# Performance work log

Measured on AMD Instinct MI355X. Metric: run time of the kernel, lower is better.

## Reference

```python
import jax, jax.numpy as jnp
import numpy as np

N = 50000
E = 1600000
D_CONTENT, D_STYLE, D_CAT = 768, 128, 32  # concat feature = 2*D_CAT = 64
H1, H2, NCLS = 64, 64, 2


def _lin_params(key, din, dout, bias=True):
    k1, k2 = jax.random.split(key)
    s = 1.0 / np.sqrt(din)
    W = jax.random.uniform(k1, (din, dout), jnp.float32, -s, s)
    b = jax.random.uniform(k2, (dout,), jnp.float32, -s, s) if bias else None
    return W, b


def setup_inputs() -> dict:
    key = jax.random.key(0)
    ks = jax.random.split(key, 16)
    x_content = jax.random.normal(ks[0], (N, D_CONTENT), jnp.float32)
    x_style = jax.random.normal(ks[1], (N, D_STYLE), jnp.float32)
    edge_index = jax.random.randint(ks[2], (2, E), 0, N, jnp.int64)
    edge_type = jax.random.randint(ks[3], (E,), 0, 4, jnp.int64)
    Wp, bp = _lin_params(ks[4], D_CONTENT, D_CAT)
    Ws, bs = _lin_params(ks[5], D_STYLE, D_CAT)
    # SAGEConv: lin_l (aggregated neighbors, has bias), lin_r (root, no bias)
    Wl1, bl1 = _lin_params(ks[6], 2 * D_CAT, H1)
    Wr1, _ = _lin_params(ks[7], 2 * D_CAT, H1, bias=False)
    Wl2, bl2 = _lin_params(ks[8], H1, H2)
    Wr2, _ = _lin_params(ks[9], H1, H2, bias=False)
    Wl3, bl3 = _lin_params(ks[10], H2, H2)
    Wr3, _ = _lin_params(ks[11], H2, H2, bias=False)
    Wo, bo = _lin_params(ks[12], H2, NCLS)
    return dict(x_content=x_content, x_style=x_style, edge_index=edge_index,
                edge_type=edge_type, Wp=Wp, bp=bp, Ws=Ws, bs=bs,
                Wl1=Wl1, bl1=bl1, Wr1=Wr1, Wl2=Wl2, bl2=bl2, Wr2=Wr2,
                Wl3=Wl3, bl3=bl3, Wr3=Wr3, Wo=Wo, bo=bo)


def _sage_conv(x, src, dst, Wl, bl, Wr):
    # mean aggregation of source-node features at destination nodes
    msg_sum = jax.ops.segment_sum(x[src], dst, num_segments=N)  # [N, d]
    deg = jax.ops.segment_sum(jnp.ones((src.shape[0],), x.dtype), dst,
                              num_segments=N)
    agg = msg_sum / jnp.maximum(deg, 1.0)[:, None]
    return agg @ Wl + bl + x @ Wr


def reference(x_content, x_style, edge_index, edge_type,
              Wp, bp, Ws, bs, Wl1, bl1, Wr1, Wl2, bl2, Wr2,
              Wl3, bl3, Wr3, Wo, bo):
    src, dst = edge_index[0], edge_index[1]
    x = jnp.concatenate([x_content @ Wp + bp, x_style @ Ws + bs], axis=1)
    x = jax.nn.relu(_sage_conv(x, src, dst, Wl1, bl1, Wr1))  # dropout = id (eval)
    x = jax.nn.relu(_sage_conv(x, src, dst, Wl2, bl2, Wr2))
    x = jax.nn.relu(_sage_conv(x, src, dst, Wl3, bl3, Wr3))
    return x @ Wo + bo
```

## Files before the change

kernel.cpp:

```cpp
#include <hip/hip_runtime.h>
#include <stdint.h>


typedef __attribute__((ext_vector_type(8))) unsigned short u16x8;
typedef __attribute__((ext_vector_type(4))) float f32x4;
typedef __attribute__((ext_vector_type(4))) unsigned int u32x4;
typedef __attribute__((ext_vector_type(2))) int i32x2;

static __device__ __forceinline__ float bf2f(unsigned short u) {
  union { unsigned int i; float f; } v;
  v.i = ((unsigned int)u) << 16;
  return v.f;
}

static __device__ __forceinline__ unsigned short f2bf(float f) {
  union { float f; unsigned int i; } v;
  v.f = f;
  unsigned int u = v.i;
  unsigned int r = (u + 0x7FFFu + ((u >> 16) & 1u)) >> 16;
  return (unsigned short)r;
}

template <bool BF>
static __device__ __forceinline__ float ldf(const void* p, long long i) {
  if (BF) return bf2f(((const unsigned short*)p)[i]);
  return ((const float*)p)[i];
}

static __device__ __forceinline__ int clampN(int v, int N) {
  return v < 0 ? 0 : (v >= N ? N - 1 : v);
}

__global__ void k_detect(const void* Wp, const int* ei, int* flags) {
  if (threadIdx.x == 0 && blockIdx.x == 0) {
    const unsigned short* w = (const unsigned short*)Wp;
    int bf = 1;
    for (int i = 0; i < 64; ++i) {
      float v = fabsf(bf2f(w[i]));
      if (!(v < 1.0f)) bf = 0;
    }
    flags[0] = bf;
    int i64 = 1;
    for (int i = 0; i < 32; ++i)
      if (ei[2 * i + 1] != 0) i64 = 0;
    flags[1] = i64;
  }
}

static __device__ __forceinline__ int edge_src(const int* ei, int e, int E,
                                               int i64) {
  return i64 ? ei[2 * (long long)e] : ei[e];
}
static __device__ __forceinline__ int edge_dst(const int* ei, int e, int E,
                                               int i64) {
  return i64 ? ei[2 * ((long long)E + e)] : ei[(long long)E + e];
}


__global__ __launch_bounds__(256) void k_pack(const int* __restrict__ ei, int E,
                                              int N, int* __restrict__ cnt,
                                              i32x2* __restrict__ pairs,
                                              const int* __restrict__ flags) {
  int e = blockIdx.x * 256 + threadIdx.x;
  if (e < E) {
    int i64 = flags[1];
    int s = clampN(edge_src(ei, e, E, i64), N);
    int d = clampN(edge_dst(ei, e, E, i64), N);
    i32x2 p;
    p[0] = s;
    p[1] = d;
    pairs[e] = p;
    atomicAdd(&cnt[d], 1);
  }
}

__global__ __launch_bounds__(256) void k_scan1(const int* __restrict__ cnt,
                                               int* __restrict__ rowptr,
                                               int* __restrict__ bsum, int N) {
  __shared__ int sh[256];
  int t = threadIdx.x;
  int base = blockIdx.x * 1024 + t * 4;
  int v0 = 0, v1 = 0, v2 = 0, v3 = 0;
  if (base + 0 < N) v0 = cnt[base + 0];
  if (base + 1 < N) v1 = cnt[base + 1];
  if (base + 2 < N) v2 = cnt[base + 2];
  if (base + 3 < N) v3 = cnt[base + 3];
  int s = v0 + v1 + v2 + v3;
  sh[t] = s;
  __syncthreads();
  int acc = s;
  for (int off = 1; off < 256; off <<= 1) {
    int x = 0;
    if (t >= off) x = sh[t - off];
    __syncthreads();
    acc += x;
    sh[t] = acc;
    __syncthreads();
  }
  int run = acc - s;
  if (base + 0 < N) rowptr[base + 0] = run;
  run += v0;
  if (base + 1 < N) rowptr[base + 1] = run;
  run += v1;
  if (base + 2 < N) rowptr[base + 2] = run;
  run += v2;
  if (base + 3 < N) rowptr[base + 3] = run;
  run += v3;
  if (t == 255) bsum[blockIdx.x] = acc;
}

__global__ void k_scan2(int* __restrict__ bsum, int nb,
                        int* __restrict__ rowptr, int N) {
  if (threadIdx.x == 0 && blockIdx.x == 0) {
    int run = 0;
    for (int i = 0; i < nb; ++i) {
      int v = bsum[i];
      bsum[i] = run;
      run += v;
    }
    rowptr[N] = run;
  }
}

__global__ __launch_bounds__(256) void k_scan3(int* __restrict__ rowptr,
                                               int* __restrict__ cursor,
                                               const int* __restrict__ bsum,
                                               int N) {
  int i = blockIdx.x * 256 + threadIdx.x;
  if (i < N) {
    int v = rowptr[i] + bsum[i >> 10];
    rowptr[i] = v;
    cursor[i] = v;
  }
}

__global__ __launch_bounds__(256) void k_scatter2(
    const i32x2* __restrict__ pairs, int E, int lo, int hi,
    int* __restrict__ cursor, int* __restrict__ colbuf) {
  int e = blockIdx.x * 256 + threadIdx.x;
  if (e < E) {
    i32x2 p2 = pairs[e];
    int d = p2[1];
    if (d >= lo && d < hi) {
      int p = atomicAdd(&cursor[d], 1);
      if (p >= 0 && p < E) colbuf[p] = p2[0];
    }
  }
}

template <bool BF>
static __device__ void project_body(const void* __restrict__ xc,
                                    const void* __restrict__ xs,
                                    const void* __restrict__ Wp,
                                    const void* __restrict__ bp,
                                    const void* __restrict__ Ws,
                                    const void* __restrict__ bs,
                                    float* __restrict__ h0, int N,
                                    float* __restrict__ lds) {
  float* xt = lds;
  unsigned int* wtb = (unsigned int*)(lds + 2 * 64 * 68);
  float* wtf = lds + 2 * 64 * 68;

  int tid = (int)threadIdx.x;
  int w = __builtin_amdgcn_readfirstlane(tid >> 6);
  int lane = tid & 63;
  int node = (int)blockIdx.x * 64 + lane;

  int sn = tid >> 2;
  int sj = tid & 3;
  int gsn = (int)blockIdx.x * 64 + sn;
  int gsnc = gsn < N ? gsn : (N - 1);

  float c[8], s[8];
#pragma unroll
  for (int r = 0; r < 8; ++r) {
    c[r] = 0.f;
    s[r] = 0.f;
  }

  u16x8 pr0 = {}, pr1 = {};
  f32x4 pf0 = {}, pf1 = {}, pf2 = {}, pf3 = {};
  u32x4 wrg = {};
  f32x4 wf0 = {}, wf1 = {};

  auto stage_load = [&](int t) {
    long long idx;
    const void* src;
    if (t < 12) {
      src = xc;
      idx = (long long)gsnc * 768 + t * 64 + 16 * sj;
    } else {
      src = xs;
      idx = (long long)gsnc * 128 + (t - 12) * 64 + 16 * sj;
    }
    if (BF) {
      const unsigned short* p = (const unsigned short*)src + idx;
      pr0 = *(const u16x8*)p;
      pr1 = *(const u16x8*)(p + 8);
    } else {
      const float* p = (const float*)src + idx;
      pf0 = *(const f32x4*)(p + 0);
      pf1 = *(const f32x4*)(p + 4);
      pf2 = *(const f32x4*)(p + 8);
      pf3 = *(const f32x4*)(p + 12);
    }
    int rowg = (t < 12) ? (t * 64 + sn) : ((t - 12) * 64 + sn);
    const void* wsrc = (t < 12) ? Wp : Ws;
    if (BF) {
      wrg = *(const u32x4*)((const unsigned int*)wsrc +
                            (long long)rowg * 16 + 4 * sj);
    } else {
      const float* p = (const float*)wsrc + (long long)rowg * 32 + 8 * sj;
      wf0 = *(const f32x4*)p;
      wf1 = *(const f32x4*)(p + 4);
    }
  };

  auto stage_write = [&](int t) {
    float* row = xt + (t & 1) * (64 * 68) + sn * 68 + 16 * sj;
    if (BF) {
      f32x4 v;
#pragma unroll
      for (int i = 0; i < 4; ++i) v[i] = bf2f(pr0[i]);
      *(f32x4*)(row + 0) = v;
#pragma unroll
      for (int i = 0; i < 4; ++i) v[i] = bf2f(pr0[4 + i]);
      *(f32x4*)(row + 4) = v;
#pragma unroll
      for (int i = 0; i < 4; ++i) v[i] = bf2f(pr1[i]);
      *(f32x4*)(row + 8) = v;
#pragma unroll
      for (int i = 0; i < 4; ++i) v[i] = bf2f(pr1[4 + i]);
      *(f32x4*)(row + 12) = v;
    } else {
      *(f32x4*)(row + 0) = pf0;
      *(f32x4*)(row + 4) = pf1;
      *(f32x4*)(row + 8) = pf2;
      *(f32x4*)(row + 12) = pf3;
    }
    if (BF) {
      *(u32x4*)(wtb + (t & 1) * (64 * 16) + sn * 16 + 4 * sj) = wrg;
    } else {
      float* wrow = wtf + (t & 1) * (64 * 32) + sn * 32 + 8 * sj;
      *(f32x4*)wrow = wf0;
      *(f32x4*)(wrow + 4) = wf1;
    }
  };

  stage_load(0);
  stage_write(0);
  __syncthreads();

#pragma unroll 1
  for (int t = 0; t < 14; ++t) {
    if (t + 1 < 14) stage_load(t + 1);

    const float* xrow = xt + (t & 1) * (64 * 68) + lane * 68;
    if (BF) {
      const unsigned int* wbase = wtb + (t & 1) * (64 * 16) + 4 * w;
      if (t < 12) {
#pragma unroll 2
        for (int k0 = 0; k0 < 64; k0 += 4) {
          f32x4 x4 = *(const f32x4*)(xrow + k0);
#pragma unroll
          for (int kk = 0; kk < 4; ++kk) {
            u32x4 wp4 = *(const u32x4*)(wbase + (k0 + kk) * 16);
#pragma unroll
            for (int p = 0; p < 4; ++p) {
              union { unsigned int i; float f; } lo, hi;
              lo.i = wp4[p] << 16;
              hi.i = wp4[p] & 0xFFFF0000u;
              c[2 * p + 0] += x4[kk] * lo.f;
              c[2 * p + 1] += x4[kk] * hi.f;
            }
          }
        }
      } else {
#pragma unroll 2
        for (int k0 = 0; k0 < 64; k0 += 4) {
          f32x4 x4 = *(const f32x4*)(xrow + k0);
#pragma unroll
          for (int kk = 0; kk < 4; ++kk) {
            u32x4 wp4 = *(const u32x4*)(wbase + (k0 + kk) * 16);
#pragma unroll
            for (int p = 0; p < 4; ++p) {
              union { unsigned int i; float f; } lo, hi;
              lo.i = wp4[p] << 16;
              hi.i = wp4[p] & 0xFFFF0000u;
              s[2 * p + 0] += x4[kk] * lo.f;
              s[2 * p + 1] += x4[kk] * hi.f;
            }
          }
        }
      }
    } else {
      const float* wbase = wtf + (t & 1) * (64 * 32) + 8 * w;
      if (t < 12) {
#pragma unroll 2
        for (int k0 = 0; k0 < 64; k0 += 4) {
          f32x4 x4 = *(const f32x4*)(xrow + k0);
#pragma unroll
          for (int kk = 0; kk < 4; ++kk) {
            const float* wr = wbase + (k0 + kk) * 32;
            f32x4 wa = *(const f32x4*)wr;
            f32x4 wb = *(const f32x4*)(wr + 4);
#pragma unroll
            for (int r = 0; r < 4; ++r) {
              c[r] += x4[kk] * wa[r];
              c[4 + r] += x4[kk] * wb[r];
            }
          }
        }
      } else {
#pragma unroll 2
        for (int k0 = 0; k0 < 64; k0 += 4) {
          f32x4 x4 = *(const f32x4*)(xrow + k0);
#pragma unroll
          for (int kk = 0; kk < 4; ++kk) {
            const float* wr = wbase + (k0 + kk) * 32;
            f32x4 wa = *(const f32x4*)wr;
            f32x4 wb = *(const f32x4*)(wr + 4);
#pragma unroll
            for (int r = 0; r < 4; ++r) {
              s[r] += x4[kk] * wa[r];
              s[4 + r] += x4[kk] * wb[r];
            }
          }
        }
      }
    }

    if (t + 1 < 14) stage_write(t + 1);
    __syncthreads();
  }

  if (node < N) {
    float* orow = h0 + (long long)node * 64;
    f32x4 v;
#pragma unroll
    for (int r = 0; r < 4; ++r) v[r] = c[r] + ldf<BF>(bp, 8 * w + r);
    *(f32x4*)(orow + 8 * w) = v;
#pragma unroll
    for (int r = 0; r < 4; ++r) v[r] = c[4 + r] + ldf<BF>(bp, 8 * w + 4 + r);
    *(f32x4*)(orow + 8 * w + 4) = v;
#pragma unroll
    for (int r = 0; r < 4; ++r) v[r] = s[r] + ldf<BF>(bs, 8 * w + r);
    *(f32x4*)(orow + 32 + 8 * w) = v;
#pragma unroll
    for (int r = 0; r < 4; ++r) v[r] = s[4 + r] + ldf<BF>(bs, 8 * w + 4 + r);
    *(f32x4*)(orow + 32 + 8 * w + 4) = v;
  }
}

__global__ __launch_bounds__(256) void k_project(
    const void* __restrict__ xc, const void* __restrict__ xs,
    const void* __restrict__ Wp, const void* __restrict__ bp,
    const void* __restrict__ Ws, const void* __restrict__ bs,
    float* __restrict__ h0, int N, const int* __restrict__ flags) {
  __shared__ float lds[2 * 64 * 68 + 2 * 64 * 32];
  if (flags[0])
    project_body<true>(xc, xs, Wp, bp, Ws, bs, h0, N, lds);
  else
    project_body<false>(xc, xs, Wp, bp, Ws, bs, h0, N, lds);
}

template <bool BF>
static __device__ void layer_body(const float* __restrict__ hin,
                                  const int* __restrict__ rowptr,
                                  const int* __restrict__ colbuf,
                                  const void* Wl, const void* bl,
                                  const void* Wr, float* __restrict__ hout,
                                  int N, int last, const void* Wo,
                                  const void* bo, void* outp) {
  int node = (int)((blockIdx.x * blockDim.x + threadIdx.x) >> 6);
  int lane = (int)(threadIdx.x & 63);
  if (node >= N) return;
  int rs = rowptr[node], re = rowptr[node + 1];
  float xself = hin[(long long)node * 64 + lane];
  float agg0 = 0.f, agg1 = 0.f, agg2 = 0.f, agg3 = 0.f;
  float agg4 = 0.f, agg5 = 0.f, agg6 = 0.f, agg7 = 0.f;
  for (int cb = rs; cb < re; cb += 64) {
    int sidx = 0;
    if (cb + lane < re) sidx = clampN(colbuf[cb + lane], N);
    int c = re - cb;
    if (c > 64) c = 64;
    int t = 0;
    for (; t + 8 <= c; t += 8) {
      int s0 = __builtin_amdgcn_readlane(sidx, t + 0);
      int s1 = __builtin_amdgcn_readlane(sidx, t + 1);
      int s2 = __builtin_amdgcn_readlane(sidx, t + 2);
      int s3 = __builtin_amdgcn_readlane(sidx, t + 3);
      int s4 = __builtin_amdgcn_readlane(sidx, t + 4);
      int s5 = __builtin_amdgcn_readlane(sidx, t + 5);
      int s6 = __builtin_amdgcn_readlane(sidx, t + 6);
      int s7 = __builtin_amdgcn_readlane(sidx, t + 7);
      float v0 = hin[(long long)s0 * 64 + lane];
      float v1 = hin[(long long)s1 * 64 + lane];
      float v2 = hin[(long long)s2 * 64 + lane];
      float v3 = hin[(long long)s3 * 64 + lane];
      float v4 = hin[(long long)s4 * 64 + lane];
      float v5 = hin[(long long)s5 * 64 + lane];
      float v6 = hin[(long long)s6 * 64 + lane];
      float v7 = hin[(long long)s7 * 64 + lane];
      agg0 += v0;
      agg1 += v1;
      agg2 += v2;
      agg3 += v3;
      agg4 += v4;
      agg5 += v5;
      agg6 += v6;
      agg7 += v7;
    }
    for (; t < c; ++t) {
      int s = __builtin_amdgcn_readlane(sidx, t);
      agg0 += hin[(long long)s * 64 + lane];
    }
  }
  float agg = ((agg0 + agg1) + (agg2 + agg3)) + ((agg4 + agg5) + (agg6 + agg7));
  int deg = re - rs;
  if (deg > 0) agg *= (1.f / (float)deg);

  float o = ldf<BF>(bl, lane);
#pragma unroll 8
  for (int d = 0; d < 64; ++d) {
    float ad = __uint_as_float(
        __builtin_amdgcn_readlane(__float_as_uint(agg), d));
    float xd = __uint_as_float(
        __builtin_amdgcn_readlane(__float_as_uint(xself), d));
    o += ad * ldf<BF>(Wl, d * 64 + lane);
    o += xd * ldf<BF>(Wr, d * 64 + lane);
  }
  o = fmaxf(o, 0.f);

  if (!last) {
    hout[(long long)node * 64 + lane] = o;
  } else {
    float c0 = o * ldf<BF>(Wo, lane * 2 + 0);
    float c1 = o * ldf<BF>(Wo, lane * 2 + 1);
    for (int off = 32; off > 0; off >>= 1) {
      c0 += __shfl_xor(c0, off, 64);
      c1 += __shfl_xor(c1, off, 64);
    }
    if (lane == 0) {
      float r0 = c0 + ldf<BF>(bo, 0);
      float r1 = c1 + ldf<BF>(bo, 1);
      if (BF) {
        unsigned short* o16 = (unsigned short*)outp;
        o16[(long long)node * 2 + 0] = f2bf(r0);
        o16[(long long)node * 2 + 1] = f2bf(r1);
      } else {
        float* o32 = (float*)outp;
        o32[(long long)node * 2 + 0] = r0;
        o32[(long long)node * 2 + 1] = r1;
      }
    }
  }
}

__global__ __launch_bounds__(256) void k_layer(
    const float* hin, const int* rowptr, const int* colbuf, const void* Wl,
    const void* bl, const void* Wr, float* hout, int N, int last,
    const void* Wo, const void* bo, void* outp, const int* __restrict__ flags) {
  if (flags[0])
    layer_body<true>(hin, rowptr, colbuf, Wl, bl, Wr, hout, N, last, Wo, bo,
                     outp);
  else
    layer_body<false>(hin, rowptr, colbuf, Wl, bl, Wr, hout, N, last, Wo, bo,
                      outp);
}


extern "C" void kernel_launch(void* const* d_in, const int* in_sizes, int n_in,
                              void* d_out, int out_size, void* d_ws,
                              size_t ws_size, hipStream_t stream) {
  const void* xc = d_in[0];
  const void* xs = d_in[1];
  const int* ei = (const int*)d_in[2];
  const void* Wp = d_in[4];
  const void* bp = d_in[5];
  const void* Ws = d_in[6];
  const void* bs = d_in[7];
  const void* Wl1 = d_in[8];
  const void* bl1 = d_in[9];
  const void* Wr1 = d_in[10];
  const void* Wl2 = d_in[11];
  const void* bl2 = d_in[12];
  const void* Wr2 = d_in[13];
  const void* Wl3 = d_in[14];
  const void* bl3 = d_in[15];
  const void* Wr3 = d_in[16];
  const void* Wo = d_in[17];
  const void* bo = d_in[18];

  int N = out_size / 2;
  int E = in_sizes[3];

  char* ws = (char*)d_ws;
  size_t off = 0;
  auto alloc = [&](size_t bytes) {
    char* p = ws + off;
    off += (bytes + 255) & ~(size_t)255;
    return p;
  };
  int* colbuf = (int*)alloc((size_t)E * 4);
  int* cnt = (int*)alloc((size_t)N * 4);
  int* rowptr = (int*)alloc((size_t)(N + 1) * 4);
  int* cursor = (int*)alloc((size_t)N * 4);
  int* bsum = (int*)alloc(4096);
  int* flags = (int*)alloc(256);
  float* h0 = (float*)alloc((size_t)N * 64 * 4);
  float* h1 = (float*)alloc((size_t)N * 64 * 4);
  (void)ws_size;
  (void)n_in;

  i32x2* pairs = (i32x2*)h0;

  k_detect<<<1, 64, 0, stream>>>(Wp, ei, flags);

  hipMemsetAsync(cnt, 0, (size_t)N * 4, stream);
  int eb = (E + 255) / 256;
  k_pack<<<eb, 256, 0, stream>>>(ei, E, N, cnt, pairs, flags);
  int sb = (N + 1023) / 1024;
  k_scan1<<<sb, 256, 0, stream>>>(cnt, rowptr, bsum, N);
  k_scan2<<<1, 64, 0, stream>>>(bsum, sb, rowptr, N);
  k_scan3<<<(N + 255) / 256, 256, 0, stream>>>(rowptr, cursor, bsum, N);

  const int NPASS = 8;
  int chunk = (N + NPASS - 1) / NPASS;
  for (int r = 0; r < NPASS; ++r) {
    int lo = r * chunk;
    int hi = lo + chunk < N ? lo + chunk : N;
    k_scatter2<<<eb, 256, 0, stream>>>(pairs, E, lo, hi, cursor, colbuf);
  }

  int pb = (N + 63) / 64;
  k_project<<<pb, 256, 0, stream>>>(xc, xs, Wp, bp, Ws, bs, h0, N, flags);

  int nb4 = (N + 3) / 4;
  k_layer<<<nb4, 256, 0, stream>>>(h0, rowptr, colbuf, Wl1, bl1, Wr1, h1, N, 0,
                                   nullptr, nullptr, nullptr, flags);
  k_layer<<<nb4, 256, 0, stream>>>(h1, rowptr, colbuf, Wl2, bl2, Wr2, h0, N, 0,
                                   nullptr, nullptr, nullptr, flags);
  k_layer<<<nb4, 256, 0, stream>>>(h0, rowptr, colbuf, Wl3, bl3, Wr3, h1, N, 1,
                                   Wo, bo, d_out, flags);
}
```

Baseline: 730.2 us.

## Split projection K-range across two blocks, widen gather unroll, halve scatter passes

```diff
diff --git a/kernel.cpp b/kernel.cpp
--- a/kernel.cpp
+++ b/kernel.cpp
@@ -152,10 +152,9 @@
 static __device__ void project_body(const void* __restrict__ xc,
                                     const void* __restrict__ xs,
                                     const void* __restrict__ Wp,
-                                    const void* __restrict__ bp,
                                     const void* __restrict__ Ws,
-                                    const void* __restrict__ bs,
-                                    float* __restrict__ h0, int N,
+                                    float* __restrict__ pout, int N,
+                                    int nb0, int tile_lo, int tile_hi,
                                     float* __restrict__ lds) {
   float* xt = lds;
   unsigned int* wtb = (unsigned int*)(lds + 2 * 64 * 68);
@@ -164,11 +163,11 @@
   int tid = (int)threadIdx.x;
   int w = __builtin_amdgcn_readfirstlane(tid >> 6);
   int lane = tid & 63;
-  int node = (int)blockIdx.x * 64 + lane;
+  int node = nb0 * 64 + lane;
 
   int sn = tid >> 2;
   int sj = tid & 3;
-  int gsn = (int)blockIdx.x * 64 + sn;
+  int gsn = nb0 * 64 + sn;
   int gsnc = gsn < N ? gsn : (N - 1);
 
   float c[8], s[8];
@@ -247,13 +246,13 @@
     }
   };
 
-  stage_load(0);
-  stage_write(0);
+  stage_load(tile_lo);
+  stage_write(tile_lo);
   __syncthreads();
 
 #pragma unroll 1
-  for (int t = 0; t < 14; ++t) {
-    if (t + 1 < 14) stage_load(t + 1);
+  for (int t = tile_lo; t < tile_hi; ++t) {
+    if (t + 1 < tile_hi) stage_load(t + 1);
 
     const float* xrow = xt + (t & 1) * (64 * 68) + lane * 68;
     if (BF) {
@@ -330,38 +329,75 @@
       }
     }
 
-    if (t + 1 < 14) stage_write(t + 1);
+    if (t + 1 < tile_hi) stage_write(t + 1);
     __syncthreads();
   }
 
   if (node < N) {
-    float* orow = h0 + (long long)node * 64;
+    float* orow = pout + (long long)node * 64;
     f32x4 v;
 #pragma unroll
-    for (int r = 0; r < 4; ++r) v[r] = c[r] + ldf<BF>(bp, 8 * w + r);
+    for (int r = 0; r < 4; ++r) v[r] = c[r];
     *(f32x4*)(orow + 8 * w) = v;
 #pragma unroll
-    for (int r = 0; r < 4; ++r) v[r] = c[4 + r] + ldf<BF>(bp, 8 * w + 4 + r);
+    for (int r = 0; r < 4; ++r) v[r] = c[4 + r];
     *(f32x4*)(orow + 8 * w + 4) = v;
 #pragma unroll
-    for (int r = 0; r < 4; ++r) v[r] = s[r] + ldf<BF>(bs, 8 * w + r);
+    for (int r = 0; r < 4; ++r) v[r] = s[r];
     *(f32x4*)(orow + 32 + 8 * w) = v;
 #pragma unroll
-    for (int r = 0; r < 4; ++r) v[r] = s[4 + r] + ldf<BF>(bs, 8 * w + 4 + r);
+    for (int r = 0; r < 4; ++r) v[r] = s[4 + r];
     *(f32x4*)(orow + 32 + 8 * w + 4) = v;
   }
 }
 
 __global__ __launch_bounds__(256) void k_project(
     const void* __restrict__ xc, const void* __restrict__ xs,
-    const void* __restrict__ Wp, const void* __restrict__ bp,
-    const void* __restrict__ Ws, const void* __restrict__ bs,
-    float* __restrict__ h0, int N, const int* __restrict__ flags) {
+    const void* __restrict__ Wp, const void* __restrict__ Ws,
+    float* __restrict__ p0, float* __restrict__ p1, int N,
+    const int* __restrict__ flags) {
   __shared__ float lds[2 * 64 * 68 + 2 * 64 * 32];
+  int b = (int)blockIdx.x;
+  int nb0 = b >> 1;
+  int half = b & 1;
+  float* pout = half ? p1 : p0;
+  int tlo = half * 7, thi = half * 7 + 7;
   if (flags[0])
-    project_body<true>(xc, xs, Wp, bp, Ws, bs, h0, N, lds);
+    project_body<true>(xc, xs, Wp, Ws, pout, N, nb0, tlo, thi, lds);
   else
-    project_body<false>(xc, xs, Wp, bp, Ws, bs, h0, N, lds);
+    project_body<false>(xc, xs, Wp, Ws, pout, N, nb0, tlo, thi, lds);
+}
+
+template <bool BF>
+static __device__ void combine_body(float* __restrict__ p0,
+                                    const float* __restrict__ p1,
+                                    const void* __restrict__ bp,
+                                    const void* __restrict__ bs, int N) {
+  long long i = (long long)blockIdx.x * 256 + threadIdx.x;
+  long long tot = (long long)N * 16;
+  if (i < tot) {
+    int oc = (int)((i & 15) * 4);
+    f32x4 a = *(f32x4*)(p0 + i * 4);
+    f32x4 b = *(const f32x4*)(p1 + i * 4);
+    f32x4 v;
+#pragma unroll
+    for (int r = 0; r < 4; ++r) {
+      int col = oc + r;
+      float bias = (col < 32) ? ldf<BF>(bp, col) : ldf<BF>(bs, col - 32);
+      v[r] = a[r] + b[r] + bias;
+    }
+    *(f32x4*)(p0 + i * 4) = v;
+  }
+}
+
+__global__ __launch_bounds__(256) void k_combine(
+    float* __restrict__ p0, const float* __restrict__ p1,
+    const void* __restrict__ bp, const void* __restrict__ bs, int N,
+    const int* __restrict__ flags) {
+  if (flags[0])
+    combine_body<true>(p0, p1, bp, bs, N);
+  else
+    combine_body<false>(p0, p1, bp, bs, N);
 }
 
 template <bool BF>
@@ -385,6 +421,48 @@
     int c = re - cb;
     if (c > 64) c = 64;
     int t = 0;
+    for (; t + 16 <= c; t += 16) {
+      int s0 = __builtin_amdgcn_readlane(sidx, t + 0);
+      int s1 = __builtin_amdgcn_readlane(sidx, t + 1);
+      int s2 = __builtin_amdgcn_readlane(sidx, t + 2);
+      int s3 = __builtin_amdgcn_readlane(sidx, t + 3);
+      int s4 = __builtin_amdgcn_readlane(sidx, t + 4);
+      int s5 = __builtin_amdgcn_readlane(sidx, t + 5);
+      int s6 = __builtin_amdgcn_readlane(sidx, t + 6);
+      int s7 = __builtin_amdgcn_readlane(sidx, t + 7);
+      int s8 = __builtin_amdgcn_readlane(sidx, t + 8);
+      int s9 = __builtin_amdgcn_readlane(sidx, t + 9);
+      int sa = __builtin_amdgcn_readlane(sidx, t + 10);
+      int sb = __builtin_amdgcn_readlane(sidx, t + 11);
+      int sc = __builtin_amdgcn_readlane(sidx, t + 12);
+      int sd = __builtin_amdgcn_readlane(sidx, t + 13);
+      int se = __builtin_amdgcn_readlane(sidx, t + 14);
+      int sf = __builtin_amdgcn_readlane(sidx, t + 15);
+      float v0 = hin[(long long)s0 * 64 + lane];
+      float v1 = hin[(long long)s1 * 64 + lane];
+      float v2 = hin[(long long)s2 * 64 + lane];
+      float v3 = hin[(long long)s3 * 64 + lane];
+      float v4 = hin[(long long)s4 * 64 + lane];
+      float v5 = hin[(long long)s5 * 64 + lane];
+      float v6 = hin[(long long)s6 * 64 + lane];
+      float v7 = hin[(long long)s7 * 64 + lane];
+      float v8 = hin[(long long)s8 * 64 + lane];
+      float v9 = hin[(long long)s9 * 64 + lane];
+      float va = hin[(long long)sa * 64 + lane];
+      float vb = hin[(long long)sb * 64 + lane];
+      float vc = hin[(long long)sc * 64 + lane];
+      float vd = hin[(long long)sd * 64 + lane];
+      float ve = hin[(long long)se * 64 + lane];
+      float vf = hin[(long long)sf * 64 + lane];
+      agg0 += v0 + v8;
+      agg1 += v1 + v9;
+      agg2 += v2 + va;
+      agg3 += v3 + vb;
+      agg4 += v4 + vc;
+      agg5 += v5 + vd;
+      agg6 += v6 + ve;
+      agg7 += v7 + vf;
+    }
     for (; t + 8 <= c; t += 8) {
       int s0 = __builtin_amdgcn_readlane(sidx, t + 0);
       int s1 = __builtin_amdgcn_readlane(sidx, t + 1);
@@ -525,7 +603,7 @@
   k_scan2<<<1, 64, 0, stream>>>(bsum, sb, rowptr, N);
   k_scan3<<<(N + 255) / 256, 256, 0, stream>>>(rowptr, cursor, bsum, N);
 
-  const int NPASS = 8;
+  const int NPASS = 4;
   int chunk = (N + NPASS - 1) / NPASS;
   for (int r = 0; r < NPASS; ++r) {
     int lo = r * chunk;
@@ -534,7 +612,9 @@
   }
 
   int pb = (N + 63) / 64;
-  k_project<<<pb, 256, 0, stream>>>(xc, xs, Wp, bp, Ws, bs, h0, N, flags);
+  k_project<<<2 * pb, 256, 0, stream>>>(xc, xs, Wp, Ws, h0, h1, N, flags);
+  int cb = (int)(((long long)N * 16 + 255) / 256);
+  k_combine<<<cb, 256, 0, stream>>>(h0, h1, bp, bs, N, flags);
 
   int nb4 = (N + 3) / 4;
   k_layer<<<nb4, 256, 0, stream>>>(h0, rowptr, colbuf, Wl1, bl1, Wr1, h1, N, 0,
```

New measurement: 721.3 us. Within noise of the previous version (-1.2%).
